# Kernel tuning notes

Measured on AMD Instinct MI355X. Metric: run time of the kernel, lower is better.

Reference implementation:

```python
import jax, jax.numpy as jnp
import numpy as np

N, E, D_IN, D_OUT = 100000, 1600000, 128, 128
EPS = 1e-12  # torch F.normalize clamp


def setup_inputs() -> dict:
    key = jax.random.key(0)
    ks = jax.random.split(key, 8)
    return {
        "x": jax.random.normal(ks[0], (N, D_IN), dtype=jnp.float32),
        "edge_src": jax.random.randint(ks[1], (E,), 0, N, dtype=jnp.int32),
        "edge_dst": jax.random.randint(ks[2], (E,), 0, N, dtype=jnp.int32),
        "edge_weight": jax.random.uniform(ks[3], (E,), dtype=jnp.float32),
        "W_l": jax.random.normal(ks[4], (D_IN, D_OUT), dtype=jnp.float32) / np.sqrt(D_IN),
        "b_l": jax.random.normal(ks[5], (D_OUT,), dtype=jnp.float32) * 0.01,
        "W_r": jax.random.normal(ks[6], (D_IN, D_OUT), dtype=jnp.float32) / np.sqrt(D_IN),
        "b_r": jax.random.normal(ks[7], (D_OUT,), dtype=jnp.float32) * 0.01,
    }


def reference(x, edge_src, edge_dst, edge_weight, W_l, b_l, W_r, b_r):
    # spmm(adj, x): weighted gather of source node features, scatter-add to targets
    agg = jax.ops.segment_sum(x[edge_src] * edge_weight[:, None], edge_dst,
                              num_segments=x.shape[0])          # [N, D_IN]
    out = agg @ W_l + b_l + (x @ W_r + b_r)                      # lin_l + lin_r (num_tgt == N)
    # L1 normalize along features (F.normalize, p=1, dim=1)
    l1 = jnp.maximum(jnp.sum(jnp.abs(out), axis=1, keepdims=True), EPS)
    return out / l1
```

## Files before the change

kernel.cpp:

```cpp
#include <hip/hip_runtime.h>
#include <hip/hip_fp16.h>


static constexpr int D = 128;
static constexpr int NB = 1024;
static constexpr int CBITS = 7;
static constexpr int CSZ = 1 << CBITS;

typedef _Float16 half8 __attribute__((ext_vector_type(8)));
typedef float f32x4 __attribute__((ext_vector_type(4)));

__global__ __launch_bounds__(256) void cvt_x_fp16(
    const float4* __restrict__ x4, __half2* __restrict__ xh2, int n4)
{
    int i = blockIdx.x * blockDim.x + threadIdx.x;
    int stride = gridDim.x * blockDim.x;
    for (; i < n4; i += stride) {
        float4 v = x4[i];
        xh2[2 * i + 0] = __floats2half2_rn(v.x, v.y);
        xh2[2 * i + 1] = __floats2half2_rn(v.z, v.w);
    }
}

__global__ __launch_bounds__(256) void wt_build(
    const float* __restrict__ Wl, const float* __restrict__ Wr,
    __half* __restrict__ wt)
{
    const int idx = blockIdx.x * blockDim.x + threadIdx.x;
    if (idx >= 128 * 256) return;
    const int c = idx >> 8;
    const int k = idx & 255;
    const float v = (k < 128) ? Wl[(size_t)k * D + c] : Wr[(size_t)(k - 128) * D + c];
    wt[(size_t)c * 256 + k] = __float2half(v);
}

__global__ __launch_bounds__(256) void coarse_count(
    const int* __restrict__ edst, int* __restrict__ ccnt, int E, int chunk)
{
    __shared__ int hist[NB];
    for (int t = threadIdx.x; t < NB; t += 256) hist[t] = 0;
    __syncthreads();
    const int beg = blockIdx.x * chunk;
    const int end = min(E, beg + chunk);
    for (int e = beg + threadIdx.x; e < end; e += 256)
        atomicAdd(&hist[edst[e] >> CBITS], 1);
    __syncthreads();
    for (int t = threadIdx.x; t < NB; t += 256) {
        const int c = hist[t];
        if (c) atomicAdd(&ccnt[t], c);
    }
}

__global__ __launch_bounds__(NB) void coarse_scan(
    const int* __restrict__ ccnt, int* __restrict__ cbase,
    int* __restrict__ ccur, int* __restrict__ offs, int N, int E)
{
    __shared__ int s[NB];
    const int t = threadIdx.x;
    const int v = ccnt[t];
    s[t] = v;
    __syncthreads();
    for (int off = 1; off < NB; off <<= 1) {
        const int u = (t >= off) ? s[t - off] : 0;
        __syncthreads();
        s[t] += u;
        __syncthreads();
    }
    const int excl = s[t] - v;
    cbase[t] = excl;
    ccur[t]  = excl;
    if (t == NB - 1) { cbase[NB] = s[t]; offs[N] = E; }
}

__global__ __launch_bounds__(256) void coarse_partition(
    const int* __restrict__ esrc, const int* __restrict__ edst,
    const float* __restrict__ ew, int* ccur,
    int2* __restrict__ cpairs, int E, int chunk)
{
    __shared__ int hist[NB];
    for (int t = threadIdx.x; t < NB; t += 256) hist[t] = 0;
    __syncthreads();
    const int beg = blockIdx.x * chunk;
    const int end = min(E, beg + chunk);
    for (int e = beg + threadIdx.x; e < end; e += 256)
        atomicAdd(&hist[edst[e] >> CBITS], 1);
    __syncthreads();
    for (int t = threadIdx.x; t < NB; t += 256) {
        const int c = hist[t];
        hist[t] = c ? atomicAdd(&ccur[t], c) : 0;
    }
    __syncthreads();
    for (int e = beg + threadIdx.x; e < end; e += 256) {
        const int d = edst[e];
        const int pos = atomicAdd(&hist[d >> CBITS], 1);
        cpairs[pos] = make_int2(((d & (CSZ - 1)) << 20) | esrc[e],
                                __float_as_int(ew[e]));
    }
}

__global__ __launch_bounds__(256) void fine_sort(
    const int2* __restrict__ cpairs, const int* __restrict__ cbase,
    int* __restrict__ offs, int2* __restrict__ pairs, int N)
{
    __shared__ int hist[CSZ];
    __shared__ int scn[CSZ];
    const int b = blockIdx.x;
    const int t = threadIdx.x;
    const int s0 = cbase[b], s1 = cbase[b + 1];
    if (t < CSZ) hist[t] = 0;
    __syncthreads();
    for (int i = s0 + t; i < s1; i += 256)
        atomicAdd(&hist[(cpairs[i].x >> 20) & (CSZ - 1)], 1);
    __syncthreads();
    if (t < CSZ) scn[t] = hist[t];
    __syncthreads();
    for (int off = 1; off < CSZ; off <<= 1) {
        int u = 0;
        if (t < CSZ && t >= off) u = scn[t - off];
        __syncthreads();
        if (t < CSZ) scn[t] += u;
        __syncthreads();
    }
    if (t < CSZ) {
        const int base = s0 + scn[t] - hist[t];
        const int node = (b << CBITS) + t;
        if (node < N) offs[node] = base;
        hist[t] = base;
    }
    __syncthreads();
    for (int i = s0 + t; i < s1; i += 256) {
        const int2 p = cpairs[i];
        const int pos = atomicAdd(&hist[(p.x >> 20) & (CSZ - 1)], 1);
        pairs[pos] = make_int2(p.x & 0xFFFFF, p.y);
    }
}

template <bool FP16X>
__global__ __launch_bounds__(256) void sage_gather(
    const void* __restrict__ xrows,
    const int2* __restrict__ pairs,
    const int* __restrict__ offs,
    void* __restrict__ agg,
    int N)
{
    int node = (blockIdx.x * blockDim.x + threadIdx.x) >> 6;
    const int lane = threadIdx.x & 63;
    if (node >= N) return;
    node = __builtin_amdgcn_readfirstlane(node);
    const int beg = offs[node];
    const int end = offs[node + 1];

    const __half2* __restrict__ xh = (const __half2*)xrows;
    const float2*  __restrict__ xf = (const float2*)xrows;

    float ax0 = 0.f, ay0 = 0.f, ax1 = 0.f, ay1 = 0.f;
    int k = beg;
    for (; k + 4 <= end; k += 4) {
        const int2 p0 = pairs[k + 0];
        const int2 p1 = pairs[k + 1];
        const int2 p2 = pairs[k + 2];
        const int2 p3 = pairs[k + 3];
        float2 v0, v1, v2, v3;
        if (FP16X) {
            v0 = __half22float2(xh[(size_t)p0.x * 64 + lane]);
            v1 = __half22float2(xh[(size_t)p1.x * 64 + lane]);
            v2 = __half22float2(xh[(size_t)p2.x * 64 + lane]);
            v3 = __half22float2(xh[(size_t)p3.x * 64 + lane]);
        } else {
            v0 = xf[(size_t)p0.x * 64 + lane];
            v1 = xf[(size_t)p1.x * 64 + lane];
            v2 = xf[(size_t)p2.x * 64 + lane];
            v3 = xf[(size_t)p3.x * 64 + lane];
        }
        const float w0 = __int_as_float(p0.y), w1 = __int_as_float(p1.y);
        const float w2 = __int_as_float(p2.y), w3 = __int_as_float(p3.y);
        ax0 = fmaf(v0.x, w0, ax0); ay0 = fmaf(v0.y, w0, ay0);
        ax1 = fmaf(v1.x, w1, ax1); ay1 = fmaf(v1.y, w1, ay1);
        ax0 = fmaf(v2.x, w2, ax0); ay0 = fmaf(v2.y, w2, ay0);
        ax1 = fmaf(v3.x, w3, ax1); ay1 = fmaf(v3.y, w3, ay1);
    }
    for (; k < end; ++k) {
        const int2 p = pairs[k];
        const float w = __int_as_float(p.y);
        float2 v;
        if (FP16X) v = __half22float2(xh[(size_t)p.x * 64 + lane]);
        else       v = xf[(size_t)p.x * 64 + lane];
        ax0 = fmaf(v.x, w, ax0); ay0 = fmaf(v.y, w, ay0);
    }
    if (FP16X) {
        ((__half2*)agg)[(size_t)node * 64 + lane] =
            __floats2half2_rn(ax0 + ax1, ay0 + ay1);
    } else {
        ((float2*)agg)[(size_t)node * 64 + lane] =
            make_float2(ax0 + ax1, ay0 + ay1);
    }
}

__global__ __launch_bounds__(256) void sage_scatter(
    const float* __restrict__ x,
    const int* __restrict__ esrc,
    const int* __restrict__ edst,
    const float* __restrict__ ew,
    float* agg, int E)
{
    const int lane = threadIdx.x & 63;
    const int warp = (blockIdx.x * blockDim.x + threadIdx.x) >> 6;
    const int nwarps = (gridDim.x * blockDim.x) >> 6;
    const float2* __restrict__ x2 = reinterpret_cast<const float2*>(x);
    for (int e = warp; e < E; e += nwarps) {
        const int s = esrc[e];
        const int d = edst[e];
        const float w = ew[e];
        const float2 xv = x2[s * 64 + lane];
        atomicAdd(&agg[d * D + lane * 2 + 0], xv.x * w);
        atomicAdd(&agg[d * D + lane * 2 + 1], xv.y * w);
    }
}

__global__ __launch_bounds__(256) void sage_linear_norm_mfma(
    const __half* __restrict__ aggh,
    const __half* __restrict__ xh,
    const __half* __restrict__ wt,
    const float* __restrict__ bl,
    const float* __restrict__ br,
    float* __restrict__ out,
    int N)
{
    __shared__ __half a_s[64][136];
    __shared__ __half w_s[128][136];
    const int tid = threadIdx.x;
    const int bn = blockIdx.x * 64;
    const int wv = tid >> 6;
    const int l  = tid & 63;
    const int lr = l & 15;
    const int lq = l >> 4;

    f32x4 acc[8];
#pragma unroll
    for (int t = 0; t < 8; ++t) acc[t] = f32x4{0.f, 0.f, 0.f, 0.f};

    const int ar  = tid >> 2;
    const int as  = (tid & 3) * 32;
    const int wr  = tid >> 1;
    const int wsg = (tid & 1) * 64;

#pragma unroll
    for (int c = 0; c < 2; ++c) {
        const __half* __restrict__ A = c ? xh : aggh;
        __syncthreads();
        {
            const int gn = bn + ar;
            half8 v0 = {}, v1 = {}, v2 = {}, v3 = {};
            if (gn < N) {
                const half8* src = reinterpret_cast<const half8*>(&A[(size_t)gn * D + as]);
                v0 = src[0]; v1 = src[1]; v2 = src[2]; v3 = src[3];
            }
            half8* dst = reinterpret_cast<half8*>(&a_s[ar][as]);
            dst[0] = v0; dst[1] = v1; dst[2] = v2; dst[3] = v3;
        }
        {
            const half8* src = reinterpret_cast<const half8*>(&wt[(size_t)wr * 256 + c * 128 + wsg]);
            half8* dst = reinterpret_cast<half8*>(&w_s[wr][wsg]);
#pragma unroll
            for (int j = 0; j < 8; ++j) dst[j] = src[j];
        }
        __syncthreads();

#pragma unroll
        for (int ks = 0; ks < 4; ++ks) {
            const int k0 = ks * 32 + lq * 8;
            const half8 af = *reinterpret_cast<const half8*>(&a_s[wv * 16 + lr][k0]);
#pragma unroll
            for (int t = 0; t < 8; ++t) {
                const half8 bf = *reinterpret_cast<const half8*>(&w_s[t * 16 + lr][k0]);
                acc[t] = __builtin_amdgcn_mfma_f32_16x16x32_f16(af, bf, acc[t], 0, 0, 0);
            }
        }
    }

    float bias[8];
#pragma unroll
    for (int t = 0; t < 8; ++t) {
        const int cidx = t * 16 + lr;
        bias[t] = bl[cidx] + br[cidx];
    }
    float v[8][4];
    float s0 = 0.f, s1 = 0.f, s2 = 0.f, s3 = 0.f;
#pragma unroll
    for (int t = 0; t < 8; ++t) {
        v[t][0] = acc[t][0] + bias[t];
        v[t][1] = acc[t][1] + bias[t];
        v[t][2] = acc[t][2] + bias[t];
        v[t][3] = acc[t][3] + bias[t];
        s0 += fabsf(v[t][0]); s1 += fabsf(v[t][1]);
        s2 += fabsf(v[t][2]); s3 += fabsf(v[t][3]);
    }
#pragma unroll
    for (int m = 1; m < 16; m <<= 1) {
        s0 += __shfl_xor(s0, m, 64);
        s1 += __shfl_xor(s1, m, 64);
        s2 += __shfl_xor(s2, m, 64);
        s3 += __shfl_xor(s3, m, 64);
    }
    const float r0 = 1.0f / fmaxf(s0, 1e-12f);
    const float r1 = 1.0f / fmaxf(s1, 1e-12f);
    const float r2 = 1.0f / fmaxf(s2, 1e-12f);
    const float r3 = 1.0f / fmaxf(s3, 1e-12f);

    const int nd0 = bn + wv * 16 + lq * 4;
#pragma unroll
    for (int r = 0; r < 4; ++r) {
        const int nd = nd0 + r;
        if (nd < N) {
            const float ri = (r == 0) ? r0 : (r == 1) ? r1 : (r == 2) ? r2 : r3;
#pragma unroll
            for (int t = 0; t < 8; ++t)
                out[(size_t)nd * D + t * 16 + lr] = v[t][r] * ri;
        }
    }
}

__global__ __launch_bounds__(256) void sage_linear_norm(
    const float* agg, const float* __restrict__ x,
    const float* __restrict__ Wl, const float* __restrict__ bl,
    const float* __restrict__ Wr, const float* __restrict__ br,
    float* out, int N)
{
    __shared__ float a_s[64][68];
    __shared__ float w_s[64][132];
    const int tid = threadIdx.x;
    const int jg = tid & 31;
    const int ng = tid >> 5;
    const int bn = blockIdx.x * 64;

    float acc[8][4];
#pragma unroll
    for (int i = 0; i < 8; ++i) {
        acc[i][0] = 0.f; acc[i][1] = 0.f; acc[i][2] = 0.f; acc[i][3] = 0.f;
    }
    const int sn  = tid >> 2;
    const int skb = (tid & 3) << 4;
    const int wr  = tid >> 5;
    const int wc  = (tid & 31) << 2;

    for (int c = 0; c < 4; ++c) {
        const float* A = (c < 2) ? agg : x;
        const float* __restrict__ W = (c < 2) ? Wl : Wr;
        const int kb = (c & 1) << 6;
        __syncthreads();
        const int gn = bn + sn;
#pragma unroll
        for (int it = 0; it < 4; ++it) {
            float4 vv = make_float4(0.f, 0.f, 0.f, 0.f);
            if (gn < N)
                vv = *reinterpret_cast<const float4*>(&A[(size_t)gn * D + kb + skb + it * 4]);
            *reinterpret_cast<float4*>(&a_s[sn][skb + it * 4]) = vv;
        }
#pragma unroll
        for (int it = 0; it < 8; ++it) {
            const int row = it * 8 + wr;
            const float4 vv = *reinterpret_cast<const float4*>(&W[(size_t)(kb + row) * D + wc]);
            *reinterpret_cast<float4*>(&w_s[row][wc]) = vv;
        }
        __syncthreads();
#pragma unroll 4
        for (int kk = 0; kk < 64; kk += 4) {
            const float4 w0 = *reinterpret_cast<const float4*>(&w_s[kk + 0][jg << 2]);
            const float4 w1 = *reinterpret_cast<const float4*>(&w_s[kk + 1][jg << 2]);
            const float4 w2 = *reinterpret_cast<const float4*>(&w_s[kk + 2][jg << 2]);
            const float4 w3 = *reinterpret_cast<const float4*>(&w_s[kk + 3][jg << 2]);
#pragma unroll
            for (int i = 0; i < 8; ++i) {
                const float4 av = *reinterpret_cast<const float4*>(&a_s[(ng << 3) + i][kk]);
                acc[i][0] = fmaf(av.w, w3.x, fmaf(av.z, w2.x, fmaf(av.y, w1.x, fmaf(av.x, w0.x, acc[i][0]))));
                acc[i][1] = fmaf(av.w, w3.y, fmaf(av.z, w2.y, fmaf(av.y, w1.y, fmaf(av.x, w0.y, acc[i][1]))));
                acc[i][2] = fmaf(av.w, w3.z, fmaf(av.z, w2.z, fmaf(av.y, w1.z, fmaf(av.x, w0.z, acc[i][2]))));
                acc[i][3] = fmaf(av.w, w3.w, fmaf(av.z, w2.w, fmaf(av.y, w1.w, fmaf(av.x, w0.w, acc[i][3]))));
            }
        }
    }
    const float4 bl4 = *reinterpret_cast<const float4*>(&bl[jg << 2]);
    const float4 br4 = *reinterpret_cast<const float4*>(&br[jg << 2]);
    const float bx = bl4.x + br4.x, by = bl4.y + br4.y,
                bz = bl4.z + br4.z, bw = bl4.w + br4.w;
#pragma unroll
    for (int i = 0; i < 8; ++i) {
        const float v0 = acc[i][0] + bx;
        const float v1 = acc[i][1] + by;
        const float v2 = acc[i][2] + bz;
        const float v3 = acc[i][3] + bw;
        float s = fabsf(v0) + fabsf(v1) + fabsf(v2) + fabsf(v3);
#pragma unroll
        for (int m = 1; m < 32; m <<= 1) s += __shfl_xor(s, m, 64);
        s = fmaxf(s, 1e-12f);
        const float r = 1.0f / s;
        const int n = bn + (ng << 3) + i;
        if (n < N) {
            const float4 o = make_float4(v0 * r, v1 * r, v2 * r, v3 * r);
            *reinterpret_cast<float4*>(&out[(size_t)n * D + (jg << 2)]) = o;
        }
    }
}

extern "C" void kernel_launch(void* const* d_in, const int* in_sizes, int n_in,
                              void* d_out, int out_size, void* d_ws, size_t ws_size,
                              hipStream_t stream) {
    const float* x    = (const float*)d_in[0];
    const int*   esrc = (const int*)  d_in[1];
    const int*   edst = (const int*)  d_in[2];
    const float* ew   = (const float*)d_in[3];
    const float* Wl   = (const float*)d_in[4];
    const float* bl   = (const float*)d_in[5];
    const float* Wr   = (const float*)d_in[6];
    const float* br   = (const float*)d_in[7];
    float* out = (float*)d_out;

    const int N = in_sizes[0] / D;
    const int E = in_sizes[1];

    auto align256 = [](size_t v) { return (v + 255) & ~size_t(255); };
    size_t off_ccnt   = 0;
    size_t off_cbase  = align256(off_ccnt   + (size_t)NB * 4);
    size_t off_ccur   = align256(off_cbase  + (size_t)(NB + 1) * 4);
    size_t off_offs   = align256(off_ccur   + (size_t)NB * 4);
    size_t off_cpairs = align256(off_offs   + (size_t)(N + 1) * 4);
    size_t off_pairs  = align256(off_cpairs + (size_t)E * 8);
    size_t off_xh     = align256(off_pairs  + (size_t)E * 8);
    size_t off_aggh   = align256(off_xh     + (size_t)N * D * 2);
    size_t off_wt     = align256(off_aggh   + (size_t)N * D * 2);
    size_t need_b     = off_xh;
    size_t need_a     = off_wt + (size_t)256 * D * 2;

    const bool fits_meta = (N <= (1 << 20)) && ((N + CSZ - 1) >> CBITS) <= NB;

    if (ws_size >= need_b && fits_meta) {
        char* ws = (char*)d_ws;
        int*  ccnt   = (int*) (ws + off_ccnt);
        int*  cbase  = (int*) (ws + off_cbase);
        int*  ccur   = (int*) (ws + off_ccur);
        int*  offs   = (int*) (ws + off_offs);
        int2* cpairs = (int2*)(ws + off_cpairs);
        int2* pairs  = (int2*)(ws + off_pairs);
        __half2* xh  = (__half2*)(ws + off_xh);
        __half*  agh = (__half*)(ws + off_aggh);
        __half*  wt  = (__half*)(ws + off_wt);

        const bool mfma = (ws_size >= need_a);
        const int chunk = (E + 255) / 256;
        const int nbu = (N + CSZ - 1) >> CBITS;

        hipMemsetAsync(ccnt, 0, (size_t)NB * 4, stream);
        if (mfma) {
            cvt_x_fp16<<<4096, 256, 0, stream>>>((const float4*)x, xh, N * (D / 4));
            wt_build<<<128, 256, 0, stream>>>(Wl, Wr, wt);
        }
        coarse_count<<<256, 256, 0, stream>>>(edst, ccnt, E, chunk);
        coarse_scan<<<1, NB, 0, stream>>>(ccnt, cbase, ccur, offs, N, E);
        coarse_partition<<<256, 256, 0, stream>>>(esrc, edst, ew, ccur, cpairs, E, chunk);
        fine_sort<<<nbu, 256, 0, stream>>>(cpairs, cbase, offs, pairs, N);

        const int gb = (N * 64 + 255) / 256;
        const int nb = (N + 63) / 64;
        if (mfma) {
            sage_gather<true ><<<gb, 256, 0, stream>>>(xh, pairs, offs, agh, N);
            sage_linear_norm_mfma<<<nb, 256, 0, stream>>>(agh, (const __half*)xh, wt,
                                                          bl, br, out, N);
        } else {
            sage_gather<false><<<gb, 256, 0, stream>>>(x, pairs, offs, out, N);
            sage_linear_norm<<<nb, 256, 0, stream>>>(out, x, Wl, bl, Wr, br, out, N);
        }
    } else {
        hipMemsetAsync(out, 0, (size_t)N * D * sizeof(float), stream);
        sage_scatter<<<2048, 256, 0, stream>>>(x, esrc, edst, ew, out, E);
        const int nb = (N + 63) / 64;
        sage_linear_norm<<<nb, 256, 0, stream>>>(out, x, Wl, bl, Wr, br, out, N);
    }
}
```

Measured before the change: 167.3 us.

## Use per-block histograms for partition offsets and split gather into two edge streams

The coarse count now writes a histogram per block instead of doing global atomics. A single-block scan turns these into per-block starting offsets, so the partition pass no longer recounts edges or does global atomics, and the memset goes away. The gather kernel now lets each half-wave take alternate edges and load 4 features per lane with wider vector loads, then combines the halves with a cross-lane shuffle. The scan walks 256 partitions serially in one block, which may add latency.

```diff
diff --git a/kernel.cpp b/kernel.cpp
--- a/kernel.cpp
+++ b/kernel.cpp
@@ -6,6 +6,7 @@
 static constexpr int NB = 1024;
 static constexpr int CBITS = 7;
 static constexpr int CSZ = 1 << CBITS;
+static constexpr int NPART = 256;
 
 typedef _Float16 half8 __attribute__((ext_vector_type(8)));
 typedef float f32x4 __attribute__((ext_vector_type(4)));
@@ -35,7 +36,7 @@
 }
 
 __global__ __launch_bounds__(256) void coarse_count(
-    const int* __restrict__ edst, int* __restrict__ ccnt, int E, int chunk)
+    const int* __restrict__ edst, int* __restrict__ bhist, int E, int chunk)
 {
     __shared__ int hist[NB];
     for (int t = threadIdx.x; t < NB; t += 256) hist[t] = 0;
@@ -45,54 +46,52 @@
     for (int e = beg + threadIdx.x; e < end; e += 256)
         atomicAdd(&hist[edst[e] >> CBITS], 1);
     __syncthreads();
-    for (int t = threadIdx.x; t < NB; t += 256) {
-        const int c = hist[t];
-        if (c) atomicAdd(&ccnt[t], c);
-    }
-}
-
-__global__ __launch_bounds__(NB) void coarse_scan(
-    const int* __restrict__ ccnt, int* __restrict__ cbase,
-    int* __restrict__ ccur, int* __restrict__ offs, int N, int E)
+    for (int t = threadIdx.x; t < NB; t += 256)
+        bhist[(size_t)blockIdx.x * NB + t] = hist[t];
+}
+
+__global__ __launch_bounds__(NB) void coarse_scan2(
+    int* __restrict__ bhist, int* __restrict__ cbase,
+    int* __restrict__ offs, int N, int E, int nparts)
 {
     __shared__ int s[NB];
     const int t = threadIdx.x;
-    const int v = ccnt[t];
-    s[t] = v;
-    __syncthreads();
+    int run = 0;
+    for (int b = 0; b < nparts; ++b) {
+        const int v = bhist[(size_t)b * NB + t];
+        bhist[(size_t)b * NB + t] = run;
+        run += v;
+    }
+    s[t] = run;
+    __syncthreads();
+    const int own = run;
     for (int off = 1; off < NB; off <<= 1) {
         const int u = (t >= off) ? s[t - off] : 0;
         __syncthreads();
         s[t] += u;
         __syncthreads();
     }
-    const int excl = s[t] - v;
+    const int excl = s[t] - own;
     cbase[t] = excl;
-    ccur[t]  = excl;
     if (t == NB - 1) { cbase[NB] = s[t]; offs[N] = E; }
+    for (int b = 0; b < nparts; ++b)
+        bhist[(size_t)b * NB + t] += excl;
 }
 
 __global__ __launch_bounds__(256) void coarse_partition(
     const int* __restrict__ esrc, const int* __restrict__ edst,
-    const float* __restrict__ ew, int* ccur,
+    const float* __restrict__ ew, const int* __restrict__ bhist,
     int2* __restrict__ cpairs, int E, int chunk)
 {
-    __shared__ int hist[NB];
-    for (int t = threadIdx.x; t < NB; t += 256) hist[t] = 0;
+    __shared__ int cur[NB];
+    for (int t = threadIdx.x; t < NB; t += 256)
+        cur[t] = bhist[(size_t)blockIdx.x * NB + t];
     __syncthreads();
     const int beg = blockIdx.x * chunk;
     const int end = min(E, beg + chunk);
-    for (int e = beg + threadIdx.x; e < end; e += 256)
-        atomicAdd(&hist[edst[e] >> CBITS], 1);
-    __syncthreads();
-    for (int t = threadIdx.x; t < NB; t += 256) {
-        const int c = hist[t];
-        hist[t] = c ? atomicAdd(&ccur[t], c) : 0;
-    }
-    __syncthreads();
     for (int e = beg + threadIdx.x; e < end; e += 256) {
         const int d = edst[e];
-        const int pos = atomicAdd(&hist[d >> CBITS], 1);
+        const int pos = atomicAdd(&cur[d >> CBITS], 1);
         cpairs[pos] = make_int2(((d & (CSZ - 1)) << 20) | esrc[e],
                                 __float_as_int(ew[e]));
     }
@@ -149,50 +148,86 @@
     node = __builtin_amdgcn_readfirstlane(node);
     const int beg = offs[node];
     const int end = offs[node + 1];
-
-    const __half2* __restrict__ xh = (const __half2*)xrows;
-    const float2*  __restrict__ xf = (const float2*)xrows;
-
-    float ax0 = 0.f, ay0 = 0.f, ax1 = 0.f, ay1 = 0.f;
+    const int sub = lane >> 5;
+    const int cl  = lane & 31;
+
+    const __half* __restrict__ xh = (const __half*)xrows;
+    const float*  __restrict__ xf = (const float*)xrows;
+
+    float a0 = 0.f, a1 = 0.f, a2 = 0.f, a3 = 0.f;
     int k = beg;
-    for (; k + 4 <= end; k += 4) {
-        const int2 p0 = pairs[k + 0];
-        const int2 p1 = pairs[k + 1];
-        const int2 p2 = pairs[k + 2];
-        const int2 p3 = pairs[k + 3];
-        float2 v0, v1, v2, v3;
+    for (; k + 8 <= end; k += 8) {
+        int s_[4]; float w_[4];
+#pragma unroll
+        for (int i = 0; i < 4; ++i) {
+            const int2 ea = pairs[k + 2 * i + 0];
+            const int2 eb = pairs[k + 2 * i + 1];
+            s_[i] = sub ? eb.x : ea.x;
+            w_[i] = __int_as_float(sub ? eb.y : ea.y);
+        }
         if (FP16X) {
-            v0 = __half22float2(xh[(size_t)p0.x * 64 + lane]);
-            v1 = __half22float2(xh[(size_t)p1.x * 64 + lane]);
-            v2 = __half22float2(xh[(size_t)p2.x * 64 + lane]);
-            v3 = __half22float2(xh[(size_t)p3.x * 64 + lane]);
+            float2 raw[4];
+#pragma unroll
+            for (int i = 0; i < 4; ++i)
+                raw[i] = *reinterpret_cast<const float2*>(&xh[(size_t)s_[i] * D + cl * 4]);
+#pragma unroll
+            for (int i = 0; i < 4; ++i) {
+                union { float2 f2; __half2 h[2]; } u;
+                u.f2 = raw[i];
+                const float2 f01 = __half22float2(u.h[0]);
+                const float2 f23 = __half22float2(u.h[1]);
+                a0 = fmaf(f01.x, w_[i], a0);
+                a1 = fmaf(f01.y, w_[i], a1);
+                a2 = fmaf(f23.x, w_[i], a2);
+                a3 = fmaf(f23.y, w_[i], a3);
+            }
         } else {
-            v0 = xf[(size_t)p0.x * 64 + lane];
-            v1 = xf[(size_t)p1.x * 64 + lane];
-            v2 = xf[(size_t)p2.x * 64 + lane];
-            v3 = xf[(size_t)p3.x * 64 + lane];
-        }
-        const float w0 = __int_as_float(p0.y), w1 = __int_as_float(p1.y);
-        const float w2 = __int_as_float(p2.y), w3 = __int_as_float(p3.y);
-        ax0 = fmaf(v0.x, w0, ax0); ay0 = fmaf(v0.y, w0, ay0);
-        ax1 = fmaf(v1.x, w1, ax1); ay1 = fmaf(v1.y, w1, ay1);
-        ax0 = fmaf(v2.x, w2, ax0); ay0 = fmaf(v2.y, w2, ay0);
-        ax1 = fmaf(v3.x, w3, ax1); ay1 = fmaf(v3.y, w3, ay1);
-    }
-    for (; k < end; ++k) {
-        const int2 p = pairs[k];
-        const float w = __int_as_float(p.y);
-        float2 v;
-        if (FP16X) v = __half22float2(xh[(size_t)p.x * 64 + lane]);
-        else       v = xf[(size_t)p.x * 64 + lane];
-        ax0 = fmaf(v.x, w, ax0); ay0 = fmaf(v.y, w, ay0);
-    }
-    if (FP16X) {
-        ((__half2*)agg)[(size_t)node * 64 + lane] =
-            __floats2half2_rn(ax0 + ax1, ay0 + ay1);
-    } else {
-        ((float2*)agg)[(size_t)node * 64 + lane] =
-            make_float2(ax0 + ax1, ay0 + ay1);
+            float4 raw[4];
+#pragma unroll
+            for (int i = 0; i < 4; ++i)
+                raw[i] = *reinterpret_cast<const float4*>(&xf[(size_t)s_[i] * D + cl * 4]);
+#pragma unroll
+            for (int i = 0; i < 4; ++i) {
+                a0 = fmaf(raw[i].x, w_[i], a0);
+                a1 = fmaf(raw[i].y, w_[i], a1);
+                a2 = fmaf(raw[i].z, w_[i], a2);
+                a3 = fmaf(raw[i].w, w_[i], a3);
+            }
+        }
+    }
+    for (int t = 0; k + t < end; ++t) {
+        if (sub == (t & 1)) {
+            const int2 p = pairs[k + t];
+            const float w = __int_as_float(p.y);
+            if (FP16X) {
+                union { float2 f2; __half2 h[2]; } u;
+                u.f2 = *reinterpret_cast<const float2*>(&xh[(size_t)p.x * D + cl * 4]);
+                const float2 f01 = __half22float2(u.h[0]);
+                const float2 f23 = __half22float2(u.h[1]);
+                a0 = fmaf(f01.x, w, a0); a1 = fmaf(f01.y, w, a1);
+                a2 = fmaf(f23.x, w, a2); a3 = fmaf(f23.y, w, a3);
+            } else {
+                const float4 v = *reinterpret_cast<const float4*>(&xf[(size_t)p.x * D + cl * 4]);
+                a0 = fmaf(v.x, w, a0); a1 = fmaf(v.y, w, a1);
+                a2 = fmaf(v.z, w, a2); a3 = fmaf(v.w, w, a3);
+            }
+        }
+    }
+    a0 += __shfl_xor(a0, 32, 64);
+    a1 += __shfl_xor(a1, 32, 64);
+    a2 += __shfl_xor(a2, 32, 64);
+    a3 += __shfl_xor(a3, 32, 64);
+
+    if (sub == 0) {
+        if (FP16X) {
+            union { __half2 h[2]; int2 i2; } u;
+            u.h[0] = __floats2half2_rn(a0, a1);
+            u.h[1] = __floats2half2_rn(a2, a3);
+            *reinterpret_cast<int2*>(&((__half*)agg)[(size_t)node * D + cl * 4]) = u.i2;
+        } else {
+            *reinterpret_cast<float4*>(&((float*)agg)[(size_t)node * D + cl * 4]) =
+                make_float4(a0, a1, a2, a3);
+        }
     }
 }
 
@@ -419,10 +454,9 @@
     const int E = in_sizes[1];
 
     auto align256 = [](size_t v) { return (v + 255) & ~size_t(255); };
-    size_t off_ccnt   = 0;
-    size_t off_cbase  = align256(off_ccnt   + (size_t)NB * 4);
-    size_t off_ccur   = align256(off_cbase  + (size_t)(NB + 1) * 4);
-    size_t off_offs   = align256(off_ccur   + (size_t)NB * 4);
+    size_t off_bhist  = 0;
+    size_t off_cbase  = align256(off_bhist  + (size_t)NPART * NB * 4);
+    size_t off_offs   = align256(off_cbase  + (size_t)(NB + 1) * 4);
     size_t off_cpairs = align256(off_offs   + (size_t)(N + 1) * 4);
     size_t off_pairs  = align256(off_cpairs + (size_t)E * 8);
     size_t off_xh     = align256(off_pairs  + (size_t)E * 8);
@@ -435,9 +469,8 @@
 
     if (ws_size >= need_b && fits_meta) {
         char* ws = (char*)d_ws;
-        int*  ccnt   = (int*) (ws + off_ccnt);
+        int*  bhist  = (int*) (ws + off_bhist);
         int*  cbase  = (int*) (ws + off_cbase);
-        int*  ccur   = (int*) (ws + off_ccur);
         int*  offs   = (int*) (ws + off_offs);
         int2* cpairs = (int2*)(ws + off_cpairs);
         int2* pairs  = (int2*)(ws + off_pairs);
@@ -446,17 +479,16 @@
         __half*  wt  = (__half*)(ws + off_wt);
 
         const bool mfma = (ws_size >= need_a);
-        const int chunk = (E + 255) / 256;
+        const int chunk = (E + NPART - 1) / NPART;
         const int nbu = (N + CSZ - 1) >> CBITS;
 
-        hipMemsetAsync(ccnt, 0, (size_t)NB * 4, stream);
         if (mfma) {
             cvt_x_fp16<<<4096, 256, 0, stream>>>((const float4*)x, xh, N * (D / 4));
             wt_build<<<128, 256, 0, stream>>>(Wl, Wr, wt);
         }
-        coarse_count<<<256, 256, 0, stream>>>(edst, ccnt, E, chunk);
-        coarse_scan<<<1, NB, 0, stream>>>(ccnt, cbase, ccur, offs, N, E);
-        coarse_partition<<<256, 256, 0, stream>>>(esrc, edst, ew, ccur, cpairs, E, chunk);
+        coarse_count<<<NPART, 256, 0, stream>>>(edst, bhist, E, chunk);
+        coarse_scan2<<<1, NB, 0, stream>>>(bhist, cbase, offs, N, E, NPART);
+        coarse_partition<<<NPART, 256, 0, stream>>>(esrc, edst, ew, bhist, cpairs, E, chunk);
         fine_sort<<<nbu, 256, 0, stream>>>(cpairs, cbase, offs, pairs, N);
 
         const int gb = (N * 64 + 255) / 256;
```

After: 234.8 us. 1.4x slower.
